# Kernel tuning notes

Measured on AMD Instinct MI355X. Metric: run time of the kernel, lower is better.

## Reference

```python
import jax, jax.numpy as jnp
import numpy as np
import math

B, H, L, S, D = 16, 10, 4096, 77, 64
N_EMB = 20            # subject tokens per instance (positions 4..23)
SHRINK = 2.0          # subj_attn_var_shrink_factor


def setup_inputs() -> dict:
    key = jax.random.key(0)
    kq, kk, kv = jax.random.split(key, 3)
    query = jax.random.normal(kq, (B, H, L, D), dtype=jnp.float32)
    k = jax.random.normal(kk, (B, H, S, D), dtype=jnp.float32)
    v = jax.random.normal(kv, (B, H, S, D), dtype=jnp.float32)
    # instance-major subject indices: every batch instance owns tokens 4..23
    idx_b = jnp.repeat(jnp.arange(B, dtype=jnp.int32), N_EMB).reshape(B, N_EMB)
    idx_n = jnp.tile(jnp.arange(4, 4 + N_EMB, dtype=jnp.int32), (B, 1))
    return {"query": query, "key": k, "value": v, "idx_b": idx_b, "idx_n": idx_n}


def _subj_attn_scales(attn_score, idx_b, idx_n, shrink_factor):
    # attn_score: [B,H,L,S] -> permute to [B,S,H,L] as in torch code
    a2 = jnp.transpose(attn_score, (0, 3, 1, 2))
    # gather subject-token attention: [N_SUB, N_EMB, H, L]
    subj = a2[idx_b, idx_n]
    n_sub, n_emb = subj.shape[0], subj.shape[1]
    subj = subj.mean(axis=2)                       # mean over heads -> [NS,NE,L]
    prob = jax.nn.softmax(subj, axis=2)            # over spatial positions
    Hs = Ws = int(math.isqrt(L))
    p3 = prob.reshape(n_sub, n_emb, Hs, Ws)        # [NS,NE,H,W]
    ys = jnp.arange(Hs, dtype=p3.dtype).reshape(1, 1, Hs, 1)
    xs = jnp.arange(Ws, dtype=p3.dtype).reshape(1, 1, 1, Ws)
    y_c = (p3 * ys).sum(axis=(2, 3))               # [NS,NE]
    x_c = (p3 * xs).sum(axis=(2, 3))
    var_y = (p3 * ys ** 2).sum(axis=(2, 3)) - y_c ** 2
    var_x = (p3 * xs ** 2).sum(axis=(2, 3)) - x_c ** 2
    s_x = jnp.sqrt(var_x) / (shrink_factor - 1.0)
    s_y = jnp.sqrt(var_y) / (shrink_factor - 1.0)
    # torch.meshgrid default is 'ij'
    X, Y = jnp.meshgrid(jnp.arange(Ws, dtype=p3.dtype), jnp.arange(Hs, dtype=p3.dtype), indexing="ij")
    X = X[:, :, None, None]
    Y = Y[:, :, None, None]
    grid = jnp.exp(-((X - x_c) ** 2 / (2 * s_x ** 2) + (Y - y_c) ** 2 / (2 * s_y ** 2)))  # [W,H,NS,NE]
    grid = grid / jax.lax.stop_gradient(grid.max())
    grid = jnp.transpose(grid, (2, 3, 0, 1)).reshape(n_sub, n_emb, 1, L)
    # scatter back into ones: [B,S,1,L]
    scales = jnp.ones((B, S, 1, L), dtype=attn_score.dtype)
    scales = scales.at[idx_b, idx_n].set(grid)
    return jnp.transpose(scales, (0, 2, 3, 1))     # [B,1,L,S]


def reference(query, key, value, idx_b, idx_n):
    scale = 1.0 / math.sqrt(query.shape[-1])
    attn_score = jnp.einsum("bhld,bhsd->bhls", query, key) * scale  # [B,H,L,S]
    scales = _subj_attn_scales(attn_score, idx_b, idx_n, SHRINK)
    attn_w = jax.nn.softmax(attn_score, axis=-1) * scales
    out = jnp.einsum("bhls,bhsd->bhld", attn_w, value)              # [B,H,L,D]
    return out
```

## Files before the change

### kernel.cpp

```cpp
#include <hip/hip_runtime.h>
#include <math.h>

#define B_ 16
#define H_ 10
#define L_ 4096
#define S_ 77
#define D_ 64
#define NE_ 20
#define NP_ (B_*NE_)
#define SHRINK_ 2.0f
#define LOG2E 1.4426950408889634f
#define SC_L2 (0.125f*LOG2E)
#define IT_ 4

typedef __bf16 bf16x8 __attribute__((ext_vector_type(8)));
typedef float  f32x4  __attribute__((ext_vector_type(4)));

static __device__ __forceinline__ unsigned short bfb(__bf16 x) {
  return __builtin_bit_cast(unsigned short, x);
}
static __device__ __forceinline__ __bf16 mkbf(unsigned short x) {
  return __builtin_bit_cast(__bf16, x);
}

__global__ __launch_bounds__(256, 3) void k1_subj(const float* __restrict__ Q,
                                                  const float* __restrict__ K,
                                                  const int* __restrict__ idxb,
                                                  const int* __restrict__ idxn,
                                                  float* __restrict__ subj) {
  __shared__ __bf16 KF[20][2][64][8];
  __shared__ float T[NE_][66];
  __shared__ int bs[NE_], ss[NE_], s_uni;
  const int i = blockIdx.y, bx = blockIdx.x;
  const int tid = threadIdx.x, lane = tid & 63, wid = tid >> 6;
  const int c = lane & 15, g = lane >> 4;
  if (tid < NE_) { bs[tid] = idxb[i*NE_ + tid]; ss[tid] = idxn[i*NE_ + tid]; }
  __syncthreads();
  if (tid == 0) { int u = 1; for (int j = 1; j < NE_; ++j) u &= (bs[j] == bs[0]); s_uni = u; }
  for (int e4 = tid; e4 < 32*160; e4 += 256) {
    int j = e4 / 160, k = (e4 - j*160) * 4;
    float4 kv = make_float4(0.f, 0.f, 0.f, 0.f);
    if (j < NE_) kv = *(const float4*)&K[(((size_t)bs[j]*H_ + (k >> 6))*S_ + ss[j])*D_ + (k & 63)];
    int ks = k >> 5, gg = (k >> 3) & 3, jj = k & 7, n = j >> 4, cc = j & 15;
    uint2 pk;
    pk.x = (unsigned)bfb((__bf16)kv.x) | ((unsigned)bfb((__bf16)kv.y) << 16);
    pk.y = (unsigned)bfb((__bf16)kv.z) | ((unsigned)bfb((__bf16)kv.w) << 16);
    *(uint2*)&KF[ks][n][gg*16 + cc][jj] = pk;
  }
  __syncthreads();
  if (!s_uni) {
    int ll = tid & 63;
    for (int ii = 0; ii < 2; ++ii) {
      int l = bx*128 + ii*64 + ll;
      for (int j = tid >> 6; j < NE_; j += 4) {
        float a = 0.f;
        for (int h = 0; h < H_; ++h) {
          const float* qp = Q + (((size_t)bs[j]*H_ + h)*L_ + l)*D_;
          const float* kp = K + (((size_t)bs[j]*H_ + h)*S_ + ss[j])*D_;
          for (int d = 0; d < 64; ++d) a += qp[d]*kp[d];
        }
        subj[(size_t)(i*NE_ + j)*L_ + l] = a * (1.0f/80.0f);
      }
    }
    return;
  }
  const int b0 = bs[0];
  #pragma unroll 1
  for (int it = 0; it < 2; ++it) {
    const int lrow = bx*128 + it*64 + wid*16 + c;
    f32x4 acc0 = {0.f,0.f,0.f,0.f}, acc1 = {0.f,0.f,0.f,0.f};
    #pragma unroll 4
    for (int ks = 0; ks < 20; ++ks) {
      const float* qp = Q + (((size_t)b0*H_ + (ks >> 1))*L_ + lrow)*D_ + (ks & 1)*32 + g*8;
      const float4 a = *(const float4*)qp;
      const float4 bq = *(const float4*)(qp + 4);
      bf16x8 af;
      af[0]=(__bf16)a.x;  af[1]=(__bf16)a.y;  af[2]=(__bf16)a.z;  af[3]=(__bf16)a.w;
      af[4]=(__bf16)bq.x; af[5]=(__bf16)bq.y; af[6]=(__bf16)bq.z; af[7]=(__bf16)bq.w;
      bf16x8 k0 = *(bf16x8*)&KF[ks][0][lane][0];
      bf16x8 k1 = *(bf16x8*)&KF[ks][1][lane][0];
      acc0 = __builtin_amdgcn_mfma_f32_16x16x32_bf16(af, k0, acc0, 0, 0, 0);
      acc1 = __builtin_amdgcn_mfma_f32_16x16x32_bf16(af, k1, acc1, 0, 0, 0);
    }
    const float sc = 1.0f/80.0f;
    #pragma unroll
    for (int r = 0; r < 4; ++r) {
      int ll = wid*16 + g*4 + r;
      T[c][ll] = acc0[r]*sc;
      if (c < 4) T[16 + c][ll] = acc1[r]*sc;
    }
    __syncthreads();
    for (int e = tid; e < NE_*64; e += 256) {
      int j = e >> 6, ll = e & 63;
      subj[(size_t)(i*NE_ + j)*L_ + bx*128 + it*64 + ll] = T[j][ll];
    }
    __syncthreads();
  }
}

__global__ __launch_bounds__(256) void k2_moments(const float* __restrict__ subj,
                                                  float* __restrict__ params) {
  const int p = blockIdx.x;
  const int tid = threadIdx.x;
  const int lane = tid & 63, wid = tid >> 6;
  const float* sp = subj + (size_t)p*L_;
  __shared__ float red[4];
  float m = -1e30f;
  for (int l = tid; l < L_; l += 256) m = fmaxf(m, sp[l]);
  #pragma unroll
  for (int s = 1; s < 64; s <<= 1) m = fmaxf(m, __shfl_xor(m, s, 64));
  if (lane == 0) red[wid] = m;
  __syncthreads();
  m = fmaxf(fmaxf(red[0], red[1]), fmaxf(red[2], red[3]));
  __syncthreads();
  float se = 0, sy = 0, sx = 0, syy = 0, sxx = 0;
  for (int l = tid; l < L_; l += 256) {
    float e = __expf(sp[l] - m);
    float y = (float)(l >> 6), x = (float)(l & 63);
    se += e; sy += e*y; sx += e*x; syy += e*y*y; sxx += e*x*x;
  }
  float vals[5] = {se, sy, sx, syy, sxx};
  #pragma unroll
  for (int q = 0; q < 5; ++q) {
    float v = vals[q];
    #pragma unroll
    for (int s = 1; s < 64; s <<= 1) v += __shfl_xor(v, s, 64);
    if (lane == 0) red[wid] = v;
    __syncthreads();
    v = red[0] + red[1] + red[2] + red[3];
    __syncthreads();
    vals[q] = v;
  }
  if (tid == 0) {
    float xc = vals[2]/vals[0], yc = vals[1]/vals[0];
    float varx = vals[4]/vals[0] - xc*xc;
    float vary = vals[3]/vals[0] - yc*yc;
    float sh = SHRINK_ - 1.0f;
    float isx = sh*sh/(2.f*varx), isy = sh*sh/(2.f*vary);
    float rx = rintf(xc), ry = rintf(yc);
    float mv = __expf(-((rx-xc)*(rx-xc)*isx + (ry-yc)*(ry-yc)*isy));
    params[p*8+0] = xc; params[p*8+1] = yc;
    params[p*8+2] = isx; params[p*8+3] = isy; params[p*8+4] = mv;
  }
}

__global__ __launch_bounds__(256) void k2b_finish(const float* __restrict__ params,
                                                  const int* __restrict__ idxb,
                                                  const int* __restrict__ idxn,
                                                  int* __restrict__ pmap,
                                                  float* __restrict__ l2invg) {
  const int tid = threadIdx.x;
  for (int e = tid; e < B_*S_; e += 256) pmap[e] = -1;
  __syncthreads();
  for (int p = tid; p < NP_; p += 256) pmap[idxb[p]*S_ + idxn[p]] = p;
  float m = 0.f;
  for (int p = tid; p < NP_; p += 256) m = fmaxf(m, params[p*8+4]);
  #pragma unroll
  for (int s = 1; s < 64; s <<= 1) m = fmaxf(m, __shfl_xor(m, s, 64));
  __shared__ float red[4];
  if ((tid & 63) == 0) red[tid >> 6] = m;
  __syncthreads();
  if (tid == 0) {
    m = fmaxf(fmaxf(red[0], red[1]), fmaxf(red[2], red[3]));
    l2invg[0] = -log2f(m);
  }
}

__global__ __launch_bounds__(256, 2) void k3_attn(const float* __restrict__ Q,
                                                  const float* __restrict__ K,
                                                  const float* __restrict__ V,
                                                  const int* __restrict__ pmap,
                                                  const float* __restrict__ params,
                                                  const float* __restrict__ l2invg,
                                                  float* __restrict__ out) {
  __shared__ __bf16 KF[2][5][64][8];
  __shared__ __bf16 VF[3][4][64][8];
  __shared__ __bf16 Wl[4][16][104];
  __shared__ float4 pp[80];
  __shared__ float  ppc[80];

  const int bh = blockIdx.y, b = bh / H_, bx = blockIdx.x;
  const int tid = threadIdx.x, lane = tid & 63, wid = tid >> 6;
  const int c = lane & 15, g = lane >> 4;

  *(uint2*)&Wl[wid][c][80 + g*4] = make_uint2(0u, 0u);

  for (int e4 = tid; e4 < 80*16; e4 += 256) {
    int s = e4 >> 4, d = (e4 & 15) * 4;
    float4 kv = make_float4(0.f, 0.f, 0.f, 0.f);
    if (s < S_) kv = *(const float4*)&K[((size_t)bh*S_ + s)*D_ + d];
    int n = s >> 4, cc = s & 15, ks = d >> 5, gg = (d >> 3) & 3, jj = d & 7;
    uint2 pk;
    pk.x = (unsigned)bfb((__bf16)kv.x) | ((unsigned)bfb((__bf16)kv.y) << 16);
    pk.y = (unsigned)bfb((__bf16)kv.z) | ((unsigned)bfb((__bf16)kv.w) << 16);
    *(uint2*)&KF[ks][n][gg*16 + cc][jj] = pk;
  }
  for (int e4 = tid; e4 < 96*16; e4 += 256) {
    int s = e4 >> 4, d = (e4 & 15) * 4;
    float4 vv = make_float4(0.f, 0.f, 0.f, 0.f);
    if (s < S_) vv = *(const float4*)&V[((size_t)bh*S_ + s)*D_ + d];
    int ks = s >> 5, gg = (s >> 3) & 3, jj = s & 7;
    int n0 = d >> 4, c0 = d & 15;
    VF[ks][n0][gg*16 + c0 + 0][jj] = (__bf16)vv.x;
    VF[ks][n0][gg*16 + c0 + 1][jj] = (__bf16)vv.y;
    VF[ks][n0][gg*16 + c0 + 2][jj] = (__bf16)vv.z;
    VF[ks][n0][gg*16 + c0 + 3][jj] = (__bf16)vv.w;
  }
  for (int s = tid; s < 80; s += 256) {
    float4 v = make_float4(0.f, 0.f, 0.f, 0.f);
    float cs = 0.f;
    if (s < S_) {
      int pid = pmap[b*S_ + s];
      if (pid >= 0) {
        v.x = params[pid*8+1];
        v.y = -params[pid*8+3]*LOG2E;
        v.z = params[pid*8+0];
        v.w = -params[pid*8+2]*LOG2E;
        cs  = l2invg[0];
      }
    }
    pp[s] = v; ppc[s] = cs;
  }
  __syncthreads();

  #pragma unroll 1
  for (int it = 0; it < IT_; ++it) {
    const int lt = bx*(64*IT_) + it*64 + wid*16;
    const float* qbase = Q + ((size_t)bh*L_ + lt + c)*D_ + g*8;
    const float4 qa0 = *(const float4*)(qbase);
    const float4 qa1 = *(const float4*)(qbase + 4);
    const float4 qc0 = *(const float4*)(qbase + 32);
    const float4 qc1 = *(const float4*)(qbase + 36);

    bf16x8 qh[2], ql[2];
    {
      float vv0[8] = {qa0.x, qa0.y, qa0.z, qa0.w, qa1.x, qa1.y, qa1.z, qa1.w};
      float vv1[8] = {qc0.x, qc0.y, qc0.z, qc0.w, qc1.x, qc1.y, qc1.z, qc1.w};
      #pragma unroll
      for (int j = 0; j < 8; ++j) {
        unsigned u0 = __float_as_uint(vv0[j]);
        qh[0][j] = mkbf((unsigned short)(u0 >> 16));
        ql[0][j] = (__bf16)(vv0[j] - __uint_as_float(u0 & 0xffff0000u));
        unsigned u1 = __float_as_uint(vv1[j]);
        qh[1][j] = mkbf((unsigned short)(u1 >> 16));
        ql[1][j] = (__bf16)(vv1[j] - __uint_as_float(u1 & 0xffff0000u));
      }
    }

    f32x4 acc[5];
    #pragma unroll
    for (int n = 0; n < 5; ++n) acc[n] = f32x4{0.f, 0.f, 0.f, 0.f};
    #pragma unroll
    for (int ks = 0; ks < 2; ++ks) {
      #pragma unroll
      for (int n = 0; n < 5; ++n) {
        bf16x8 kf = *(bf16x8*)&KF[ks][n][lane][0];
        acc[n] = __builtin_amdgcn_mfma_f32_16x16x32_bf16(qh[ks], kf, acc[n], 0, 0, 0);
        acc[n] = __builtin_amdgcn_mfma_f32_16x16x32_bf16(ql[ks], kf, acc[n], 0, 0, 0);
      }
    }
    if (c >= 13) {
      #pragma unroll
      for (int r = 0; r < 4; ++r) acc[4][r] = -1e30f;
    }
    #pragma unroll
    for (int n = 0; n < 5; ++n)
      #pragma unroll
      for (int r = 0; r < 4; ++r) acc[n][r] = __builtin_amdgcn_exp2f(acc[n][r] * SC_L2);
    float sm[4];
    #pragma unroll
    for (int r = 0; r < 4; ++r) {
      float s0 = acc[0][r] + acc[1][r] + acc[2][r] + acc[3][r] + acc[4][r];
      #pragma unroll
      for (int s = 1; s < 16; s <<= 1) s0 += __shfl_xor(s0, s, 64);
      sm[r] = __builtin_amdgcn_rcpf(s0);
    }
    const float Xf = (float)(bx*IT_ + it);
    const float Yb = (float)(wid*16 + g*4);
    #pragma unroll
    for (int n = 0; n < 5; ++n) {
      const float4 sp4 = pp[16*n + c];
      const float tx = Xf - sp4.z;
      const float Cn = fmaf(tx*tx, sp4.w, ppc[16*n + c]);
      #pragma unroll
      for (int r = 0; r < 4; ++r) {
        float t = (Yb + (float)r) - sp4.x;
        float gm = __builtin_amdgcn_exp2f(fmaf(t*t, sp4.y, Cn));
        float w = acc[n][r] * gm * sm[r];
        Wl[wid][g*4 + r][16*n + c] = (__bf16)w;
      }
    }
    f32x4 pacc[4];
    #pragma unroll
    for (int n = 0; n < 4; ++n) pacc[n] = f32x4{0.f, 0.f, 0.f, 0.f};
    #pragma unroll
    for (int ks = 0; ks < 3; ++ks) {
      bf16x8 wf = *(bf16x8*)&Wl[wid][c][ks*32 + g*8];
      #pragma unroll
      for (int n = 0; n < 4; ++n) {
        bf16x8 vf = *(bf16x8*)&VF[ks][n][lane][0];
        pacc[n] = __builtin_amdgcn_mfma_f32_16x16x32_bf16(wf, vf, pacc[n], 0, 0, 0);
      }
    }
    float* ob = out + ((size_t)bh*L_ + lt + g*4)*D_ + c;
    #pragma unroll
    for (int r = 0; r < 4; ++r)
      #pragma unroll
      for (int n = 0; n < 4; ++n) ob[(size_t)r*D_ + 16*n] = pacc[n][r];
  }
}

extern "C" void kernel_launch(void* const* d_in, const int* in_sizes, int n_in,
                              void* d_out, int out_size, void* d_ws, size_t ws_size,
                              hipStream_t stream) {
  const float* Q  = (const float*)d_in[0];
  const float* Kp = (const float*)d_in[1];
  const float* Vp = (const float*)d_in[2];
  const int* idxb = (const int*)d_in[3];
  const int* idxn = (const int*)d_in[4];
  float* out = (float*)d_out;

  char* w = (char*)d_ws;
  float* params = (float*)w;
  float* l2invg = params + NP_*8;
  int* pmap = (int*)(l2invg + 4);
  size_t head = (size_t)(NP_*8 + 4)*sizeof(float) + (size_t)B_*S_*sizeof(int);
  head = (head + 255) & ~(size_t)255;
  float* subj;
  if (ws_size >= head + (size_t)NP_*L_*sizeof(float))
    subj = (float*)(w + head);
  else
    subj = out;

  k1_subj<<<dim3(L_/128, B_), 256, 0, stream>>>(Q, Kp, idxb, idxn, subj);
  k2_moments<<<NP_, 256, 0, stream>>>(subj, params);
  k2b_finish<<<1, 256, 0, stream>>>(params, idxb, idxn, pmap, l2invg);
  k3_attn<<<dim3(L_/(64*IT_), B_*H_), 256, 0, stream>>>(Q, Kp, Vp, pmap, params, l2invg, out);
}
```

Baseline: 136.0 us.

## Drop split-bf16 Q for QK^T, double-buffer weights, unroll by two

Removes the hi/lo bf16 split of Q so QK^T takes one MFMA per tile instead of two. It also doubles the iterations per block, double-buffers the per-wave weight tile in LDS, and unrolls the loop by two so consecutive iterations can overlap. The main risk is lower accuracy in the attention scores, since Q is now rounded straight to bf16. More LDS use and half as many blocks may reduce occupancy or parallelism.

```diff
diff --git a/kernel.cpp b/kernel.cpp
--- a/kernel.cpp
+++ b/kernel.cpp
@@ -11,7 +11,7 @@
 #define SHRINK_ 2.0f
 #define LOG2E 1.4426950408889634f
 #define SC_L2 (0.125f*LOG2E)
-#define IT_ 4
+#define IT_ 8
 
 typedef __bf16 bf16x8 __attribute__((ext_vector_type(8)));
 typedef float  f32x4  __attribute__((ext_vector_type(4)));
@@ -175,7 +175,7 @@
                                                   float* __restrict__ out) {
   __shared__ __bf16 KF[2][5][64][8];
   __shared__ __bf16 VF[3][4][64][8];
-  __shared__ __bf16 Wl[4][16][104];
+  __shared__ __bf16 Wl[2][4][16][104];
   __shared__ float4 pp[80];
   __shared__ float  ppc[80];
 
@@ -183,7 +183,8 @@
   const int tid = threadIdx.x, lane = tid & 63, wid = tid >> 6;
   const int c = lane & 15, g = lane >> 4;
 
-  *(uint2*)&Wl[wid][c][80 + g*4] = make_uint2(0u, 0u);
+  *(uint2*)&Wl[0][wid][c][80 + g*4] = make_uint2(0u, 0u);
+  *(uint2*)&Wl[1][wid][c][80 + g*4] = make_uint2(0u, 0u);
 
   for (int e4 = tid; e4 < 80*16; e4 += 256) {
     int s = e4 >> 4, d = (e4 & 15) * 4;
@@ -223,29 +224,19 @@
   }
   __syncthreads();
 
-  #pragma unroll 1
-  for (int it = 0; it < IT_; ++it) {
+  auto body = [&](int it) {
+    const int wb = it & 1;
     const int lt = bx*(64*IT_) + it*64 + wid*16;
     const float* qbase = Q + ((size_t)bh*L_ + lt + c)*D_ + g*8;
-    const float4 qa0 = *(const float4*)(qbase);
-    const float4 qa1 = *(const float4*)(qbase + 4);
-    const float4 qc0 = *(const float4*)(qbase + 32);
-    const float4 qc1 = *(const float4*)(qbase + 36);
-
-    bf16x8 qh[2], ql[2];
-    {
-      float vv0[8] = {qa0.x, qa0.y, qa0.z, qa0.w, qa1.x, qa1.y, qa1.z, qa1.w};
-      float vv1[8] = {qc0.x, qc0.y, qc0.z, qc0.w, qc1.x, qc1.y, qc1.z, qc1.w};
-      #pragma unroll
-      for (int j = 0; j < 8; ++j) {
-        unsigned u0 = __float_as_uint(vv0[j]);
-        qh[0][j] = mkbf((unsigned short)(u0 >> 16));
-        ql[0][j] = (__bf16)(vv0[j] - __uint_as_float(u0 & 0xffff0000u));
-        unsigned u1 = __float_as_uint(vv1[j]);
-        qh[1][j] = mkbf((unsigned short)(u1 >> 16));
-        ql[1][j] = (__bf16)(vv1[j] - __uint_as_float(u1 & 0xffff0000u));
-      }
-    }
+    const float4 a0 = *(const float4*)(qbase);
+    const float4 a1 = *(const float4*)(qbase + 4);
+    const float4 b0 = *(const float4*)(qbase + 32);
+    const float4 b1 = *(const float4*)(qbase + 36);
+    bf16x8 qf[2];
+    qf[0][0]=(__bf16)a0.x; qf[0][1]=(__bf16)a0.y; qf[0][2]=(__bf16)a0.z; qf[0][3]=(__bf16)a0.w;
+    qf[0][4]=(__bf16)a1.x; qf[0][5]=(__bf16)a1.y; qf[0][6]=(__bf16)a1.z; qf[0][7]=(__bf16)a1.w;
+    qf[1][0]=(__bf16)b0.x; qf[1][1]=(__bf16)b0.y; qf[1][2]=(__bf16)b0.z; qf[1][3]=(__bf16)b0.w;
+    qf[1][4]=(__bf16)b1.x; qf[1][5]=(__bf16)b1.y; qf[1][6]=(__bf16)b1.z; qf[1][7]=(__bf16)b1.w;
 
     f32x4 acc[5];
     #pragma unroll
@@ -255,8 +246,7 @@
       #pragma unroll
       for (int n = 0; n < 5; ++n) {
         bf16x8 kf = *(bf16x8*)&KF[ks][n][lane][0];
-        acc[n] = __builtin_amdgcn_mfma_f32_16x16x32_bf16(qh[ks], kf, acc[n], 0, 0, 0);
-        acc[n] = __builtin_amdgcn_mfma_f32_16x16x32_bf16(ql[ks], kf, acc[n], 0, 0, 0);
+        acc[n] = __builtin_amdgcn_mfma_f32_16x16x32_bf16(qf[ks], kf, acc[n], 0, 0, 0);
       }
     }
     if (c >= 13) {
@@ -287,7 +277,7 @@
         float t = (Yb + (float)r) - sp4.x;
         float gm = __builtin_amdgcn_exp2f(fmaf(t*t, sp4.y, Cn));
         float w = acc[n][r] * gm * sm[r];
-        Wl[wid][g*4 + r][16*n + c] = (__bf16)w;
+        Wl[wb][wid][g*4 + r][16*n + c] = (__bf16)w;
       }
     }
     f32x4 pacc[4];
@@ -295,7 +285,7 @@
     for (int n = 0; n < 4; ++n) pacc[n] = f32x4{0.f, 0.f, 0.f, 0.f};
     #pragma unroll
     for (int ks = 0; ks < 3; ++ks) {
-      bf16x8 wf = *(bf16x8*)&Wl[wid][c][ks*32 + g*8];
+      bf16x8 wf = *(bf16x8*)&Wl[wb][wid][c][ks*32 + g*8];
       #pragma unroll
       for (int n = 0; n < 4; ++n) {
         bf16x8 vf = *(bf16x8*)&VF[ks][n][lane][0];
@@ -307,6 +297,12 @@
     for (int r = 0; r < 4; ++r)
       #pragma unroll
       for (int n = 0; n < 4; ++n) ob[(size_t)r*D_ + 16*n] = pacc[n][r];
+  };
+
+  #pragma unroll 1
+  for (int it2 = 0; it2 < IT_; it2 += 2) {
+    body(it2);
+    body(it2 + 1);
   }
 }
 
```

After: 131.7 us. -3.2%, faster.

## Drop split-bf16 Q precision and process two 16-row tiles per wave

Applied to the files above, without the earlier changes.

Replaces the hi/lo bf16 split of Q, which cost two MFMAs per K chunk, with a single bf16 conversion. Each wave now handles 32 rows as two independent 16-row tiles, so there is more MFMA work in flight and the K and V fragment loads are reused across both tiles. Iterations per block drop and launch bounds relax to allow more registers. Rounding Q straight to bf16 loses precision in the attention scores, which could push results past tolerance.

```diff
diff --git a/kernel.cpp b/kernel.cpp
--- a/kernel.cpp
+++ b/kernel.cpp
@@ -11,7 +11,7 @@
 #define SHRINK_ 2.0f
 #define LOG2E 1.4426950408889634f
 #define SC_L2 (0.125f*LOG2E)
-#define IT_ 4
+#define IT_ 2
 
 typedef __bf16 bf16x8 __attribute__((ext_vector_type(8)));
 typedef float  f32x4  __attribute__((ext_vector_type(4)));
@@ -166,7 +166,7 @@
   }
 }
 
-__global__ __launch_bounds__(256, 2) void k3_attn(const float* __restrict__ Q,
+__global__ __launch_bounds__(256, 1) void k3_attn(const float* __restrict__ Q,
                                                   const float* __restrict__ K,
                                                   const float* __restrict__ V,
                                                   const int* __restrict__ pmap,
@@ -175,7 +175,7 @@
                                                   float* __restrict__ out) {
   __shared__ __bf16 KF[2][5][64][8];
   __shared__ __bf16 VF[3][4][64][8];
-  __shared__ __bf16 Wl[4][16][104];
+  __shared__ __bf16 Wl[4][2][16][104];
   __shared__ float4 pp[80];
   __shared__ float  ppc[80];
 
@@ -183,7 +183,8 @@
   const int tid = threadIdx.x, lane = tid & 63, wid = tid >> 6;
   const int c = lane & 15, g = lane >> 4;
 
-  *(uint2*)&Wl[wid][c][80 + g*4] = make_uint2(0u, 0u);
+  *(uint2*)&Wl[wid][0][c][80 + g*4] = make_uint2(0u, 0u);
+  *(uint2*)&Wl[wid][1][c][80 + g*4] = make_uint2(0u, 0u);
 
   for (int e4 = tid; e4 < 80*16; e4 += 256) {
     int s = e4 >> 4, d = (e4 & 15) * 4;
@@ -225,88 +226,101 @@
 
   #pragma unroll 1
   for (int it = 0; it < IT_; ++it) {
-    const int lt = bx*(64*IT_) + it*64 + wid*16;
-    const float* qbase = Q + ((size_t)bh*L_ + lt + c)*D_ + g*8;
-    const float4 qa0 = *(const float4*)(qbase);
-    const float4 qa1 = *(const float4*)(qbase + 4);
-    const float4 qc0 = *(const float4*)(qbase + 32);
-    const float4 qc1 = *(const float4*)(qbase + 36);
-
-    bf16x8 qh[2], ql[2];
-    {
-      float vv0[8] = {qa0.x, qa0.y, qa0.z, qa0.w, qa1.x, qa1.y, qa1.z, qa1.w};
-      float vv1[8] = {qc0.x, qc0.y, qc0.z, qc0.w, qc1.x, qc1.y, qc1.z, qc1.w};
-      #pragma unroll
-      for (int j = 0; j < 8; ++j) {
-        unsigned u0 = __float_as_uint(vv0[j]);
-        qh[0][j] = mkbf((unsigned short)(u0 >> 16));
-        ql[0][j] = (__bf16)(vv0[j] - __uint_as_float(u0 & 0xffff0000u));
-        unsigned u1 = __float_as_uint(vv1[j]);
-        qh[1][j] = mkbf((unsigned short)(u1 >> 16));
-        ql[1][j] = (__bf16)(vv1[j] - __uint_as_float(u1 & 0xffff0000u));
-      }
-    }
-
-    f32x4 acc[5];
-    #pragma unroll
-    for (int n = 0; n < 5; ++n) acc[n] = f32x4{0.f, 0.f, 0.f, 0.f};
+    const int lt = bx*(128*IT_) + it*128 + wid*32;
+    bf16x8 qf[2][2];
+    #pragma unroll
+    for (int t = 0; t < 2; ++t) {
+      const float* qbase = Q + ((size_t)bh*L_ + lt + t*16 + c)*D_ + g*8;
+      #pragma unroll
+      for (int ks = 0; ks < 2; ++ks) {
+        const float4 a0 = *(const float4*)(qbase + ks*32);
+        const float4 a1 = *(const float4*)(qbase + ks*32 + 4);
+        qf[t][ks][0]=(__bf16)a0.x; qf[t][ks][1]=(__bf16)a0.y;
+        qf[t][ks][2]=(__bf16)a0.z; qf[t][ks][3]=(__bf16)a0.w;
+        qf[t][ks][4]=(__bf16)a1.x; qf[t][ks][5]=(__bf16)a1.y;
+        qf[t][ks][6]=(__bf16)a1.z; qf[t][ks][7]=(__bf16)a1.w;
+      }
+    }
+
+    f32x4 acc[2][5];
+    #pragma unroll
+    for (int t = 0; t < 2; ++t)
+      #pragma unroll
+      for (int n = 0; n < 5; ++n) acc[t][n] = f32x4{0.f, 0.f, 0.f, 0.f};
     #pragma unroll
     for (int ks = 0; ks < 2; ++ks) {
       #pragma unroll
       for (int n = 0; n < 5; ++n) {
         bf16x8 kf = *(bf16x8*)&KF[ks][n][lane][0];
-        acc[n] = __builtin_amdgcn_mfma_f32_16x16x32_bf16(qh[ks], kf, acc[n], 0, 0, 0);
-        acc[n] = __builtin_amdgcn_mfma_f32_16x16x32_bf16(ql[ks], kf, acc[n], 0, 0, 0);
+        acc[0][n] = __builtin_amdgcn_mfma_f32_16x16x32_bf16(qf[0][ks], kf, acc[0][n], 0, 0, 0);
+        acc[1][n] = __builtin_amdgcn_mfma_f32_16x16x32_bf16(qf[1][ks], kf, acc[1][n], 0, 0, 0);
       }
     }
     if (c >= 13) {
       #pragma unroll
-      for (int r = 0; r < 4; ++r) acc[4][r] = -1e30f;
-    }
-    #pragma unroll
-    for (int n = 0; n < 5; ++n)
-      #pragma unroll
-      for (int r = 0; r < 4; ++r) acc[n][r] = __builtin_amdgcn_exp2f(acc[n][r] * SC_L2);
-    float sm[4];
-    #pragma unroll
-    for (int r = 0; r < 4; ++r) {
-      float s0 = acc[0][r] + acc[1][r] + acc[2][r] + acc[3][r] + acc[4][r];
-      #pragma unroll
-      for (int s = 1; s < 16; s <<= 1) s0 += __shfl_xor(s0, s, 64);
-      sm[r] = __builtin_amdgcn_rcpf(s0);
-    }
-    const float Xf = (float)(bx*IT_ + it);
-    const float Yb = (float)(wid*16 + g*4);
+      for (int t = 0; t < 2; ++t)
+        #pragma unroll
+        for (int r = 0; r < 4; ++r) acc[t][4][r] = -1e30f;
+    }
+    #pragma unroll
+    for (int t = 0; t < 2; ++t)
+      #pragma unroll
+      for (int n = 0; n < 5; ++n)
+        #pragma unroll
+        for (int r = 0; r < 4; ++r)
+          acc[t][n][r] = __builtin_amdgcn_exp2f(acc[t][n][r] * SC_L2);
+    float sm[2][4];
+    #pragma unroll
+    for (int t = 0; t < 2; ++t)
+      #pragma unroll
+      for (int r = 0; r < 4; ++r) {
+        float s0 = acc[t][0][r] + acc[t][1][r] + acc[t][2][r] + acc[t][3][r] + acc[t][4][r];
+        #pragma unroll
+        for (int s = 1; s < 16; s <<= 1) s0 += __shfl_xor(s0, s, 64);
+        sm[t][r] = __builtin_amdgcn_rcpf(s0);
+      }
+    const float Xf = (float)(bx*2*IT_ + it*2 + (wid >> 1));
+    const float Yb0 = (float)((wid & 1)*32 + g*4);
     #pragma unroll
     for (int n = 0; n < 5; ++n) {
       const float4 sp4 = pp[16*n + c];
       const float tx = Xf - sp4.z;
       const float Cn = fmaf(tx*tx, sp4.w, ppc[16*n + c]);
       #pragma unroll
-      for (int r = 0; r < 4; ++r) {
-        float t = (Yb + (float)r) - sp4.x;
-        float gm = __builtin_amdgcn_exp2f(fmaf(t*t, sp4.y, Cn));
-        float w = acc[n][r] * gm * sm[r];
-        Wl[wid][g*4 + r][16*n + c] = (__bf16)w;
-      }
-    }
-    f32x4 pacc[4];
-    #pragma unroll
-    for (int n = 0; n < 4; ++n) pacc[n] = f32x4{0.f, 0.f, 0.f, 0.f};
+      for (int t = 0; t < 2; ++t) {
+        #pragma unroll
+        for (int r = 0; r < 4; ++r) {
+          float ty = (Yb0 + (float)(t*16 + r)) - sp4.x;
+          float gm = __builtin_amdgcn_exp2f(fmaf(ty*ty, sp4.y, Cn));
+          float w = acc[t][n][r] * gm * sm[t][r];
+          Wl[wid][t][g*4 + r][16*n + c] = (__bf16)w;
+        }
+      }
+    }
+    f32x4 pacc[2][4];
+    #pragma unroll
+    for (int t = 0; t < 2; ++t)
+      #pragma unroll
+      for (int n = 0; n < 4; ++n) pacc[t][n] = f32x4{0.f, 0.f, 0.f, 0.f};
     #pragma unroll
     for (int ks = 0; ks < 3; ++ks) {
-      bf16x8 wf = *(bf16x8*)&Wl[wid][c][ks*32 + g*8];
+      bf16x8 wf0 = *(bf16x8*)&Wl[wid][0][c][ks*32 + g*8];
+      bf16x8 wf1 = *(bf16x8*)&Wl[wid][1][c][ks*32 + g*8];
       #pragma unroll
       for (int n = 0; n < 4; ++n) {
         bf16x8 vf = *(bf16x8*)&VF[ks][n][lane][0];
-        pacc[n] = __builtin_amdgcn_mfma_f32_16x16x32_bf16(wf, vf, pacc[n], 0, 0, 0);
-      }
-    }
-    float* ob = out + ((size_t)bh*L_ + lt + g*4)*D_ + c;
-    #pragma unroll
-    for (int r = 0; r < 4; ++r)
-      #pragma unroll
-      for (int n = 0; n < 4; ++n) ob[(size_t)r*D_ + 16*n] = pacc[n][r];
+        pacc[0][n] = __builtin_amdgcn_mfma_f32_16x16x32_bf16(wf0, vf, pacc[0][n], 0, 0, 0);
+        pacc[1][n] = __builtin_amdgcn_mfma_f32_16x16x32_bf16(wf1, vf, pacc[1][n], 0, 0, 0);
+      }
+    }
+    #pragma unroll
+    for (int t = 0; t < 2; ++t) {
+      float* ob = out + ((size_t)bh*L_ + lt + t*16 + g*4)*D_ + c;
+      #pragma unroll
+      for (int r = 0; r < 4; ++r)
+        #pragma unroll
+        for (int n = 0; n < 4; ++n) ob[(size_t)r*D_ + 16*n] = pacc[t][n][r];
+    }
   }
 }
 
@@ -335,5 +349,5 @@
   k1_subj<<<dim3(L_/128, B_), 256, 0, stream>>>(Q, Kp, idxb, idxn, subj);
   k2_moments<<<NP_, 256, 0, stream>>>(subj, params);
   k2b_finish<<<1, 256, 0, stream>>>(params, idxb, idxn, pmap, l2invg);
-  k3_attn<<<dim3(L_/(64*IT_), B_*H_), 256, 0, stream>>>(Q, Kp, Vp, pmap, params, l2invg, out);
-}
+  k3_attn<<<dim3(L_/(128*IT_), B_*H_), 256, 0, stream>>>(Q, Kp, Vp, pmap, params, l2invg, out);
+}
```

Result: slower. 149.7 us (+10.1%).
